# Optimization experiments

Measured on AMD Instinct MI355X. Metric: run time of the kernel, lower is better.

The kernel has to match this reference:

```python
import jax, jax.numpy as jnp
import numpy as np
from jax import lax

# Static module configuration (mirrors init_kwargs)
L = 64
KH, KW = 4, 7          # kernel_size (h, w), h = w // 2 + 1
DH, DW = 1, 1          # kernel_dilation
EXCLUSIVE = True
RECEP_H = (KH - 1) * DH + 1
RECEP_W = (KW - 1) * DW + 1
BATCH, IN_F, OUT_F = 4096, 64, 64


def _autoregressive_mask():
    # netket MaskedConv2D mask: full rows above the last; last row only sees
    # columns strictly left of center (exclusive=True).
    m = np.ones((KH, KW, 1, 1), np.float32)
    m[-1, KW // 2 + (0 if EXCLUSIVE else 1):, :, :] = 0.0
    return jnp.asarray(m)


def setup_inputs() -> dict:
    key = jax.random.key(0)
    k1, k2, k3, k4 = jax.random.split(key, 4)
    inputs = jax.random.normal(k1, (BATCH, IN_F), jnp.float32)
    cache = jax.random.normal(k2, (BATCH, RECEP_H, L, IN_F), jnp.float32)
    kernel = jax.random.normal(k3, (KH, KW, IN_F, OUT_F), jnp.float32) * 0.05
    bias = jax.random.normal(k4, (OUT_F,), jnp.float32) * 0.05
    return {"inputs": inputs, "cache": cache, "kernel": kernel,
            "bias": bias, "index": 1000}


def reference(inputs, cache, kernel, bias, index):
    batch, in_f = inputs.shape
    kernel = kernel * _autoregressive_mask()  # masked kernel, as at init

    index_w = index % L
    index_w_in = (index - int(EXCLUSIVE)) % L
    inp4 = inputs[:, None, None, :]  # (B, 1, 1, F)

    def _add(c):
        # -1 row start: jax wraps negative starts -> write into last cache row
        return lax.dynamic_update_slice(c, inp4, (0, -1, index_w_in, 0))

    def _shift(c):
        # shift rows up, zero-fill new last row
        return jnp.pad(c[:, 1:, :, :], ((0, 0), (0, 1), (0, 0), (0, 0)))

    cache_new_row = jnp.where(index_w_in == 0, _add(_shift(cache)), _shift(_add(cache)))
    cache_new = jnp.where(index_w == 0, cache_new_row, _add(cache))
    cache = jnp.where(index - int(EXCLUSIVE) >= 0, cache_new, cache)

    # pad width for 'SAME'-style receptive field, then slice the window at index_w
    padded = jnp.pad(cache, ((0, 0), (0, 0),
                             (KW // 2 * DW, (KW - 1) // 2 * DW), (0, 0)))
    window = lax.dynamic_slice(padded, (0, 0, index_w, 0),
                               (batch, RECEP_H, RECEP_W, in_f))  # (B, rh, rw, F)

    y = lax.conv_general_dilated(window, kernel, window_strides=(1, 1),
                                 padding='VALID', rhs_dilation=(DH, DW),
                                 dimension_numbers=('NHWC', 'HWIO', 'NHWC'))
    y = y + bias  # (B, 1, 1, OUT_F)
    return y[:, 0, 0, :], cache
```

## Files before the change

### kernel.cpp

```cpp
#include <hip/hip_runtime.h>

#define NB_CONV 256
#define NB_COPY 1792
#define NTHR 256

typedef float f4 __attribute__((ext_vector_type(4)));

__global__ __launch_bounds__(256)
void fmc_fused(const float* __restrict__ inputs,
               const float* __restrict__ cache,
               const float* __restrict__ wk,
               const float* __restrict__ bias,
               const int* __restrict__ idxp,
               float* __restrict__ y_out,
               float* __restrict__ cache_out)
{
    const int idx = idxp[0];
    int iw = idx % 64;        if (iw < 0)  iw += 64;
    int iwi = (idx - 1) % 64; if (iwi < 0) iwi += 64;
    const bool upd = (idx - 1) >= 0;
    const int tid = threadIdx.x;

    if (blockIdx.x < NB_CONV) {
        __shared__ float Ws[64][68];
        __shared__ float Xs[64][18];
        const int bbase = blockIdx.x * 16;
        const int fog = tid & 15;
        const int bp  = tid >> 4;

        float acc[2][4];
        if (tid < 128) {
            const f4 bv = *(const f4*)(bias + (fog << 2));
            acc[0][0]=bv.x; acc[0][1]=bv.y; acc[0][2]=bv.z; acc[0][3]=bv.w;
            acc[1][0]=bv.x; acc[1][1]=bv.y; acc[1][2]=bv.z; acc[1][3]=bv.w;
        }

        for (int kh = 0; kh < 4; ++kh) {
            for (int kw = 0; kw < 7; ++kw) {
                if (kh == 3 && kw >= 3) break;
                const int col = iw - 3 + kw;
                int kind;
                int hs = kh;
                if (col < 0 || col >= 64) kind = 0;
                else if (!upd) kind = 2;
                else if (iw != 0) kind = (kh == 3 && col == iwi) ? 1 : 2;
                else if (iwi != 0) {
                    if (kh == 3) kind = 0;
                    else if (kh == 2 && col == iwi) kind = 1;
                    else { kind = 2; hs = kh + 1; }
                } else {
                    if (kh == 3) kind = (col == 0) ? 1 : 0;
                    else { kind = 2; hs = kh + 1; }
                }

                __syncthreads();
                const float* wt = wk + (kh * 7 + kw) * 4096;
                #pragma unroll
                for (int i = 0; i < 4; ++i) {
                    const int f4i = tid + (i << 8);
                    const int ci = f4i >> 4;
                    const int fo = (f4i & 15) << 2;
                    *(f4*)&Ws[ci][fo] = *(const f4*)(wt + ci * 64 + fo);
                }
                {
                    const int bl = tid >> 4;
                    const int c4i = (tid & 15) << 2;
                    f4 v = (f4)(0.f);
                    if (kind == 1)
                        v = *(const f4*)(inputs + (bbase + bl) * 64 + c4i);
                    else if (kind == 2)
                        v = *(const f4*)(cache + ((((bbase + bl) << 2) + hs) * 64 + col) * 64 + c4i);
                    Xs[c4i + 0][bl] = v.x;
                    Xs[c4i + 1][bl] = v.y;
                    Xs[c4i + 2][bl] = v.z;
                    Xs[c4i + 3][bl] = v.w;
                }
                __syncthreads();

                if (tid < 128) {
                    #pragma unroll 16
                    for (int ci = 0; ci < 64; ++ci) {
                        const f4 w = *(const f4*)&Ws[ci][fog << 2];
                        const float2 x = *(const float2*)&Xs[ci][bp << 1];
                        acc[0][0] = fmaf(x.x, w.x, acc[0][0]);
                        acc[0][1] = fmaf(x.x, w.y, acc[0][1]);
                        acc[0][2] = fmaf(x.x, w.z, acc[0][2]);
                        acc[0][3] = fmaf(x.x, w.w, acc[0][3]);
                        acc[1][0] = fmaf(x.y, w.x, acc[1][0]);
                        acc[1][1] = fmaf(x.y, w.y, acc[1][1]);
                        acc[1][2] = fmaf(x.y, w.z, acc[1][2]);
                        acc[1][3] = fmaf(x.y, w.w, acc[1][3]);
                    }
                }
            }
        }
        if (tid < 128) {
            float* y0 = y_out + (bbase + (bp << 1)) * 64 + (fog << 2);
            *(f4*)y0        = (f4){acc[0][0], acc[0][1], acc[0][2], acc[0][3]};
            *(f4*)(y0 + 64) = (f4){acc[1][0], acc[1][1], acc[1][2], acc[1][3]};
        }
    } else {
        const f4* __restrict__ c4 = (const f4*)cache;
        const f4* __restrict__ i4 = (const f4*)inputs;
        f4* __restrict__ o4 = (f4*)cache_out;
        const int t0 = (blockIdx.x - NB_CONV) * NTHR + tid;
        const int stride = NB_COPY * NTHR;
        const int total = 4096 * 4096;
        if (!upd) {
            for (int i = t0; i < total; i += stride)
                __builtin_nontemporal_store(c4[i], o4 + i);
        } else if (iw != 0) {
            const int target = 3 * 1024 + iwi * 16;
            for (int i = t0; i < total; i += stride) {
                const int r = i & 4095;
                const f4* src = c4 + i;
                if ((r & ~15) == target)
                    src = i4 + ((i >> 12) << 4) + (r & 15);
                __builtin_nontemporal_store(*src, o4 + i);
            }
        } else if (iwi != 0) {
            for (int i = t0; i < total; i += stride) {
                const int r = i & 4095;
                const int h = r >> 10;
                f4 v = (f4)(0.f);
                if (h == 2 && ((r >> 4) & 63) == iwi) v = i4[((i >> 12) << 4) + (r & 15)];
                else if (h < 3) v = c4[i + 1024];
                __builtin_nontemporal_store(v, o4 + i);
            }
        } else {
            for (int i = t0; i < total; i += stride) {
                const int r = i & 4095;
                const int h = r >> 10;
                f4 v = (f4)(0.f);
                if (h == 3) { if (((r >> 4) & 63) == 0) v = i4[((i >> 12) << 4) + (r & 15)]; }
                else v = c4[i + 1024];
                __builtin_nontemporal_store(v, o4 + i);
            }
        }
    }
}

extern "C" void kernel_launch(void* const* d_in, const int* in_sizes, int n_in,
                              void* d_out, int out_size, void* d_ws, size_t ws_size,
                              hipStream_t stream) {
    const float* inputs = (const float*)d_in[0];
    const float* cache  = (const float*)d_in[1];
    const float* wk     = (const float*)d_in[2];
    const float* bias   = (const float*)d_in[3];
    const int*   idxp   = (const int*)d_in[4];
    float* y_out = (float*)d_out;
    float* cache_out = (float*)d_out + 4096 * 64;
    fmc_fused<<<NB_CONV + NB_COPY, NTHR, 0, stream>>>(inputs, cache, wk, bias, idxp,
                                                      y_out, cache_out);
}
```

Before: 104.2 us.

## Replace static copy-block split with atomic work-stealing chunk queue

```diff
diff --git a/kernel.cpp b/kernel.cpp
--- a/kernel.cpp
+++ b/kernel.cpp
@@ -1,8 +1,11 @@
 #include <hip/hip_runtime.h>
 
 #define NB_CONV 256
-#define NB_COPY 1792
+#define NB_TOTAL 1792
 #define NTHR 256
+#define CHUNK_F4 1024
+#define NCHUNK 16384
+#define TOTAL_F4 (4096 * 4096)
 
 typedef float f4 __attribute__((ext_vector_type(4)));
 
@@ -13,7 +16,8 @@
                const float* __restrict__ bias,
                const int* __restrict__ idxp,
                float* __restrict__ y_out,
-               float* __restrict__ cache_out)
+               float* __restrict__ cache_out,
+               unsigned int* __restrict__ ctr)
 {
     const int idx = idxp[0];
     int iw = idx % 64;        if (iw < 0)  iw += 64;
@@ -99,42 +103,59 @@
             *(f4*)y0        = (f4){acc[0][0], acc[0][1], acc[0][2], acc[0][3]};
             *(f4*)(y0 + 64) = (f4){acc[1][0], acc[1][1], acc[1][2], acc[1][3]};
         }
-    } else {
+    }
+
+    {
         const f4* __restrict__ c4 = (const f4*)cache;
         const f4* __restrict__ i4 = (const f4*)inputs;
         f4* __restrict__ o4 = (f4*)cache_out;
-        const int t0 = (blockIdx.x - NB_CONV) * NTHR + tid;
-        const int stride = NB_COPY * NTHR;
-        const int total = 4096 * 4096;
-        if (!upd) {
-            for (int i = t0; i < total; i += stride)
-                __builtin_nontemporal_store(c4[i], o4 + i);
-        } else if (iw != 0) {
-            const int target = 3 * 1024 + iwi * 16;
-            for (int i = t0; i < total; i += stride) {
-                const int r = i & 4095;
-                const f4* src = c4 + i;
-                if ((r & ~15) == target)
-                    src = i4 + ((i >> 12) << 4) + (r & 15);
-                __builtin_nontemporal_store(*src, o4 + i);
-            }
-        } else if (iwi != 0) {
-            for (int i = t0; i < total; i += stride) {
-                const int r = i & 4095;
-                const int h = r >> 10;
-                f4 v = (f4)(0.f);
-                if (h == 2 && ((r >> 4) & 63) == iwi) v = i4[((i >> 12) << 4) + (r & 15)];
-                else if (h < 3) v = c4[i + 1024];
-                __builtin_nontemporal_store(v, o4 + i);
-            }
-        } else {
-            for (int i = t0; i < total; i += stride) {
-                const int r = i & 4095;
-                const int h = r >> 10;
-                f4 v = (f4)(0.f);
-                if (h == 3) { if (((r >> 4) & 63) == 0) v = i4[((i >> 12) << 4) + (r & 15)]; }
-                else v = c4[i + 1024];
-                __builtin_nontemporal_store(v, o4 + i);
+        const int lane = tid & 63;
+        const int caseid = !upd ? 0 : (iw != 0 ? 1 : (iwi != 0 ? 2 : 3));
+        const int targetA = 3072 + (iwi << 4);
+
+        while (true) {
+            int c;
+            if (lane == 0) c = (int)atomicAdd(ctr, 1u);
+            c = __shfl(c, 0);
+            if (c >= NCHUNK) break;
+            const int base = c << 10;
+
+            if (caseid == 0) {
+                #pragma unroll 4
+                for (int it = 0; it < CHUNK_F4 / 64; ++it) {
+                    const int i = base + (it << 6) + lane;
+                    __builtin_nontemporal_store(c4[i], o4 + i);
+                }
+            } else if (caseid == 1) {
+                #pragma unroll 4
+                for (int it = 0; it < CHUNK_F4 / 64; ++it) {
+                    const int i = base + (it << 6) + lane;
+                    const int r = i & 4095;
+                    const f4* src = ((r & 4080) == targetA)
+                                    ? (i4 + ((i >> 12) << 4) + (r & 15))
+                                    : (c4 + i);
+                    __builtin_nontemporal_store(*src, o4 + i);
+                }
+            } else if (caseid == 2) {
+                for (int it = 0; it < CHUNK_F4 / 64; ++it) {
+                    const int i = base + (it << 6) + lane;
+                    const int r = i & 4095;
+                    const int h = r >> 10, w = (r >> 4) & 63;
+                    f4 v = (f4)(0.f);
+                    if (h == 2 && w == iwi) v = i4[((i >> 12) << 4) + (r & 15)];
+                    else if (h < 3) v = c4[i + 1024];
+                    __builtin_nontemporal_store(v, o4 + i);
+                }
+            } else {
+                for (int it = 0; it < CHUNK_F4 / 64; ++it) {
+                    const int i = base + (it << 6) + lane;
+                    const int r = i & 4095;
+                    const int h = r >> 10, w = (r >> 4) & 63;
+                    f4 v = (f4)(0.f);
+                    if (h == 3) { if (w == 0) v = i4[((i >> 12) << 4) + (r & 15)]; }
+                    else v = c4[i + 1024];
+                    __builtin_nontemporal_store(v, o4 + i);
+                }
             }
         }
     }
@@ -150,6 +171,9 @@
     const int*   idxp   = (const int*)d_in[4];
     float* y_out = (float*)d_out;
     float* cache_out = (float*)d_out + 4096 * 64;
-    fmc_fused<<<NB_CONV + NB_COPY, NTHR, 0, stream>>>(inputs, cache, wk, bias, idxp,
-                                                      y_out, cache_out);
+    unsigned int* ctr = (unsigned int*)d_ws;
+
+    hipMemsetAsync(ctr, 0, sizeof(unsigned int), stream);
+    fmc_fused<<<NB_TOTAL, NTHR, 0, stream>>>(inputs, cache, wk, bias, idxp,
+                                             y_out, cache_out, ctr);
 }
```

After: 290.9 us. 179% more time.
